# Optimization experiments

Hardware: AMD Instinct MI355X
Metric: run time of the kernel (lower is better)

Reference implementation:

```python
import jax, jax.numpy as jnp
import numpy as np

B, C_IN, C_OUT, DIRS, H, W = 16, 32, 32, 2, 64, 64


def setup_inputs() -> dict:
    key = jax.random.key(0)
    kx, kw = jax.random.split(key)
    x = jax.random.normal(kx, (B, C_IN, DIRS, H, W), dtype=jnp.float32)
    # xavier_normal_ on weight [O, C, C]: fan_in = C*C, fan_out = O*C
    std = float(np.sqrt(2.0 / (C_IN * C_IN + C_OUT * C_IN)))
    weight = jax.random.normal(kw, (C_OUT, C_IN, C_IN), dtype=jnp.float32) * std
    bias = jnp.zeros((C_OUT,), dtype=jnp.float32)
    return {"x": x, "weight": weight, "bias": bias}


def reference(x, weight, bias):
    # x: [B, C_in, dirs, H, W] real angles; z = exp(i*x)
    z = jax.lax.complex(jnp.cos(x), jnp.sin(x))  # complex64 [B,C,D,H,W]
    Wc = weight.astype(jnp.complex64)            # [O, C, C]
    # Per-pixel bilinear form: oc[b,o,d,h,w] = sum_{c,e} z[b,c] W[o,c,e] z[b,e]
    # (equivalent to the original full matmul + diagonal extraction)
    oc = jnp.einsum('oce,bcdhw,bedhw->bodhw', Wc, z, z)
    out = jnp.arctan2(oc.imag, oc.real)          # torch.angle
    return out + bias[None, :, None, None, None]
```

## Files before the change

kernel.cpp:

```cpp
#include <hip/hip_runtime.h>
#include <math.h>

typedef float        f32x2 __attribute__((ext_vector_type(2)));
typedef float        f32x4 __attribute__((ext_vector_type(4)));
typedef _Float16     f16x2 __attribute__((ext_vector_type(2)));
typedef _Float16     f16x8 __attribute__((ext_vector_type(8)));
typedef unsigned int u32;
typedef unsigned int u32x4 __attribute__((ext_vector_type(4)));

#define HW_    4096
#define CH_STR 8192
#define B_STR  262144
#define NPIX   131072
#define NKSTEP 20
#define NSLICE 80
#define NCT    84
#define NBEL   (NKSTEP*2*2*64*8)

#define WSCALE 512.0f
#define USCALE 1024.0f


__global__ void prep(const float* __restrict__ w,
                     _Float16* __restrict__ bfr,
                     u32* __restrict__ ct) {
    int idx = blockIdx.x * 256 + threadIdx.x;
    if (idx < NBEL) {
        int j    =  idx & 7;
        int lane = (idx >> 3) & 63;
        int frag = (idx >> 9) & 3;
        int ks   =  idx >> 11;
        int var  = frag >> 1;
        int oh   = frag & 1;
        int k = ks * 32 + ((lane >> 4) << 3) + j;
        int c = 0, base = 0;
        for (; c < 32; ++c) { int rl = 8 * ((c >> 3) + 1); if (k < base + rl) break; base += rl; }
        int e = k - base;
        int o = oh * 16 + (lane & 15);
        float v = 0.0f;
        if (e <= c)
            v = (e == c) ? w[o * 1024 + c * 33]
                         : (w[o * 1024 + c * 32 + e] + w[o * 1024 + e * 32 + c]);
        v *= WSCALE;
        _Float16 h = (_Float16)v;
        if (var) h = (_Float16)(v - (float)h);
        bfr[idx] = h;
    } else if (idx < NBEL + NCT) {
        int s = idx - NBEL;
        u32 v = 0;
        if (s < NSLICE) {
            int k = s * 8, c = 0, base = 0;
            for (; c < 32; ++c) { int rl = 8 * ((c >> 3) + 1); if (k < base + rl) break; base += rl; }
            v = ((u32)(c * 8) << 16) | (u32)((k - base) * 4);
        }
        ct[s] = v;
    }
}

#define TPB   256
#define TSTR  132

__device__ __forceinline__ f16x8 pack8(u32 a, u32 b, u32 c, u32 d) {
    u32x4 t = {a, b, c, d};
    return __builtin_bit_cast(f16x8, t);
}
__device__ __forceinline__ u32 pkrtz_u(float a, float b) {
    return __builtin_bit_cast(u32, __builtin_amdgcn_cvt_pkrtz(a, b));
}

__global__ __launch_bounds__(TPB, 4) void mfma_bilinear(
    const float* __restrict__ x,
    const _Float16* __restrict__ bfr,
    const u32* __restrict__ ct,
    const float* __restrict__ bias,
    float* __restrict__ out)
{
    __shared__ float trig[64 * TSTR];

    const int lane = threadIdx.x & 63;
    const int wv   = threadIdx.x >> 6;
    const int lg   = lane >> 4;
    const int lidm = lane & 15;
    const int P0   = blockIdx.x * 64;
    const int b    = P0 >> 13;
    const int d    = (P0 >> 12) & 1;
    const int hw0  = P0 & 4095;
    const int obase = b * B_STR + d * HW_ + hw0;

    const int px = wv * 16 + lidm;
    float* tp = trig + px * TSTR;
    const char* tb = (const char*)tp;

    #pragma unroll
    for (int m = 0; m < 8; ++m) {
        int c = lg * 8 + m;
        float xv = x[obase + px + c * CH_STR];
        float s, co; __sincosf(xv, &s, &co);
        *(f32x2*)(tp + 2 * c) = (f32x2){co * USCALE, s * USCALE};
        tp[64 + c] = co;
        tp[96 + c] = s;
    }

    f32x4 acc_r[2] = {{0.f,0.f,0.f,0.f}, {0.f,0.f,0.f,0.f}};
    f32x4 acc_i[2] = {{0.f,0.f,0.f,0.f}, {0.f,0.f,0.f,0.f}};

    const char* ubp = (const char*)bfr;
    const char* uct = (const char*)ct;
    const int lo16 = lane * 16;
    const int lg4  = lg * 4;

#define LDB(OFF)      (*(const f16x8*)(ubp + lo16 + (OFF)))
#define LDCT(OFF)     (*(const u32*)(uct + lg4 + (OFF)))
#define LOAD_TRIG(ST, CS, CE0, CE1, SE0, SE1) do { \
    const u32 st_ = (ST); \
    const int cB = (int)(st_ >> 16), eB = (int)(st_ & 0xffffu); \
    CS  = *(const f32x2*)(tb + cB); \
    CE0 = *(const f32x4*)(tb + 256 + eB); \
    CE1 = *(const f32x4*)(tb + 272 + eB); \
    SE0 = *(const f32x4*)(tb + 384 + eB); \
    SE1 = *(const f32x4*)(tb + 400 + eB); \
} while (0)

#define COMPUTE_STEP(CS, CE0, CE1, SE0, SE1, BH0, BH1, BL0, BL1) do { \
    const float ccs = (CS)[0]; \
    const float scs = (CS)[1]; \
    u32 hr[4], hi[4], lr[4], li[4]; \
    _Pragma("unroll") \
    for (int p = 0; p < 4; ++p) { \
        const float cea = (2*p     < 4) ? (CE0)[2*p]     : (CE1)[2*p - 4]; \
        const float sea = (2*p     < 4) ? (SE0)[2*p]     : (SE1)[2*p - 4]; \
        const float ceb = (2*p + 1 < 4) ? (CE0)[2*p + 1] : (CE1)[2*p - 3]; \
        const float seb = (2*p + 1 < 4) ? (SE0)[2*p + 1] : (SE1)[2*p - 3]; \
        const float ur0 = fmaf(ccs, cea, -(scs * sea)); \
        const float ui0 = fmaf(ccs, sea,   scs * cea); \
        const float ur1 = fmaf(ccs, ceb, -(scs * seb)); \
        const float ui1 = fmaf(ccs, seb,   scs * ceb); \
        hr[p] = pkrtz_u(ur0, ur1); \
        hi[p] = pkrtz_u(ui0, ui1); \
        const f16x2 h2r = __builtin_bit_cast(f16x2, hr[p]); \
        const f16x2 h2i = __builtin_bit_cast(f16x2, hi[p]); \
        lr[p] = pkrtz_u(ur0 - (float)h2r[0], ur1 - (float)h2r[1]); \
        li[p] = pkrtz_u(ui0 - (float)h2i[0], ui1 - (float)h2i[1]); \
    } \
    const f16x8 ahr = pack8(hr[0], hr[1], hr[2], hr[3]); \
    const f16x8 ahi = pack8(hi[0], hi[1], hi[2], hi[3]); \
    const f16x8 alr = pack8(lr[0], lr[1], lr[2], lr[3]); \
    const f16x8 ali = pack8(li[0], li[1], li[2], li[3]); \
    acc_r[0] = __builtin_amdgcn_mfma_f32_16x16x32_f16(ahr, BH0, acc_r[0], 0, 0, 0); \
    acc_i[0] = __builtin_amdgcn_mfma_f32_16x16x32_f16(ahi, BH0, acc_i[0], 0, 0, 0); \
    acc_r[1] = __builtin_amdgcn_mfma_f32_16x16x32_f16(ahr, BH1, acc_r[1], 0, 0, 0); \
    acc_i[1] = __builtin_amdgcn_mfma_f32_16x16x32_f16(ahi, BH1, acc_i[1], 0, 0, 0); \
    acc_r[0] = __builtin_amdgcn_mfma_f32_16x16x32_f16(ahr, BL0, acc_r[0], 0, 0, 0); \
    acc_i[0] = __builtin_amdgcn_mfma_f32_16x16x32_f16(ahi, BL0, acc_i[0], 0, 0, 0); \
    acc_r[1] = __builtin_amdgcn_mfma_f32_16x16x32_f16(ahr, BL1, acc_r[1], 0, 0, 0); \
    acc_i[1] = __builtin_amdgcn_mfma_f32_16x16x32_f16(ahi, BL1, acc_i[1], 0, 0, 0); \
    acc_r[0] = __builtin_amdgcn_mfma_f32_16x16x32_f16(alr, BH0, acc_r[0], 0, 0, 0); \
    acc_i[0] = __builtin_amdgcn_mfma_f32_16x16x32_f16(ali, BH0, acc_i[0], 0, 0, 0); \
    acc_r[1] = __builtin_amdgcn_mfma_f32_16x16x32_f16(alr, BH1, acc_r[1], 0, 0, 0); \
    acc_i[1] = __builtin_amdgcn_mfma_f32_16x16x32_f16(ali, BH1, acc_i[1], 0, 0, 0); \
} while (0)

    f16x8 bh0 = LDB(0), bh1 = LDB(1024), bl0 = LDB(2048), bl1 = LDB(3072);
    f32x2 cs; f32x4 ce0, ce1, se0, se1;
    LOAD_TRIG(LDCT(0), cs, ce0, ce1, se0, se1);
    u32 stN = LDCT(16);
    ubp += 4096;

    #pragma unroll 4
    for (int ks = 0; ks < NKSTEP - 1; ++ks) {
        f16x8 nbh0 = LDB(0), nbh1 = LDB(1024), nbl0 = LDB(2048), nbl1 = LDB(3072);
        f32x2 ncs; f32x4 nce0, nce1, nse0, nse1;
        LOAD_TRIG(stN, ncs, nce0, nce1, nse0, nse1);
        u32 stN2 = LDCT(32);

        COMPUTE_STEP(cs, ce0, ce1, se0, se1, bh0, bh1, bl0, bl1);

        bh0 = nbh0; bh1 = nbh1; bl0 = nbl0; bl1 = nbl1;
        cs = ncs; ce0 = nce0; ce1 = nce1; se0 = nse0; se1 = nse1;
        stN = stN2;
        ubp += 4096; uct += 16;
    }
    COMPUTE_STEP(cs, ce0, ce1, se0, se1, bh0, bh1, bl0, bl1);

    #pragma unroll
    for (int oh = 0; oh < 2; ++oh) {
        const int o = oh * 16 + lidm;
        const float bo = bias[o];
        #pragma unroll
        for (int q = 0; q < 4; ++q) {
            const int pxr = wv * 16 + lg * 4 + q;
            out[obase + pxr + o * CH_STR] = atan2f(acc_i[oh][q], acc_r[oh][q]) + bo;
        }
    }
#undef LDB
#undef LDCT
#undef LOAD_TRIG
#undef COMPUTE_STEP
}

extern "C" void kernel_launch(void* const* d_in, const int* in_sizes, int n_in,
                              void* d_out, int out_size, void* d_ws, size_t ws_size,
                              hipStream_t stream) {
    const float* x    = (const float*)d_in[0];
    const float* w    = (const float*)d_in[1];
    const float* bias = (const float*)d_in[2];
    float* out        = (float*)d_out;
    _Float16* bfr = (_Float16*)d_ws;
    u32*      ct  = (u32*)((char*)d_ws + 81920);

    {
        int n = NBEL + NCT;
        prep<<<(n + 255) / 256, 256, 0, stream>>>(w, bfr, ct);
    }
    {
        int grid = NPIX / 64;
        mfma_bilinear<<<grid, TPB, 0, stream>>>(x, bfr, ct, bias, out);
    }
}
```

Measured before the change: 53.58 us.

## Pack triangular weight rows in 4-wide chunks and compact the trig LDS table

```diff
diff --git a/kernel.cpp b/kernel.cpp
--- a/kernel.cpp
+++ b/kernel.cpp
@@ -6,16 +6,17 @@
 typedef _Float16     f16x2 __attribute__((ext_vector_type(2)));
 typedef _Float16     f16x8 __attribute__((ext_vector_type(8)));
 typedef unsigned int u32;
+typedef unsigned int u32x2 __attribute__((ext_vector_type(2)));
 typedef unsigned int u32x4 __attribute__((ext_vector_type(4)));
 
 #define HW_    4096
 #define CH_STR 8192
 #define B_STR  262144
 #define NPIX   131072
-#define NKSTEP 20
-#define NSLICE 80
-#define NCT    84
-#define NBEL   (NKSTEP*2*2*64*8)
+#define NKSTEP 18
+#define NSLICE 72
+#define NCT2   76
+#define NBEL   (NKSTEP*4*64*8)
 
 #define WSCALE 512.0f
 #define USCALE 1024.0f
@@ -23,7 +24,7 @@
 
 __global__ void prep(const float* __restrict__ w,
                      _Float16* __restrict__ bfr,
-                     u32* __restrict__ ct) {
+                     u32* __restrict__ ct2) {
     int idx = blockIdx.x * 256 + threadIdx.x;
     if (idx < NBEL) {
         int j    =  idx & 7;
@@ -34,7 +35,7 @@
         int oh   = frag & 1;
         int k = ks * 32 + ((lane >> 4) << 3) + j;
         int c = 0, base = 0;
-        for (; c < 32; ++c) { int rl = 8 * ((c >> 3) + 1); if (k < base + rl) break; base += rl; }
+        for (; c < 32; ++c) { int rl = ((c >> 2) + 1) << 2; if (k < base + rl) break; base += rl; }
         int e = k - base;
         int o = oh * 16 + (lane & 15);
         float v = 0.0f;
@@ -45,20 +46,21 @@
         _Float16 h = (_Float16)v;
         if (var) h = (_Float16)(v - (float)h);
         bfr[idx] = h;
-    } else if (idx < NBEL + NCT) {
-        int s = idx - NBEL;
+    } else if (idx < NBEL + 2 * NCT2) {
+        int t = idx - NBEL;
+        int s = t >> 1, half = t & 1;
         u32 v = 0;
         if (s < NSLICE) {
-            int k = s * 8, c = 0, base = 0;
-            for (; c < 32; ++c) { int rl = 8 * ((c >> 3) + 1); if (k < base + rl) break; base += rl; }
-            v = ((u32)(c * 8) << 16) | (u32)((k - base) * 4);
+            int k = s * 8 + half * 4, c = 0, base = 0;
+            for (; c < 32; ++c) { int rl = ((c >> 2) + 1) << 2; if (k < base + rl) break; base += rl; }
+            v = ((u32)(c * 8) << 16) | (u32)((k - base) * 8);
         }
-        ct[s] = v;
+        ct2[t] = v;
     }
 }
 
 #define TPB   256
-#define TSTR  132
+#define TSTR  67
 
 __device__ __forceinline__ f16x8 pack8(u32 a, u32 b, u32 c, u32 d) {
     u32x4 t = {a, b, c, d};
@@ -68,10 +70,10 @@
     return __builtin_bit_cast(u32, __builtin_amdgcn_cvt_pkrtz(a, b));
 }
 
-__global__ __launch_bounds__(TPB, 4) void mfma_bilinear(
+__global__ __launch_bounds__(TPB, 8) void mfma_bilinear(
     const float* __restrict__ x,
     const _Float16* __restrict__ bfr,
-    const u32* __restrict__ ct,
+    const u32* __restrict__ ct2,
     const float* __restrict__ bias,
     float* __restrict__ out)
 {
@@ -96,41 +98,41 @@
         int c = lg * 8 + m;
         float xv = x[obase + px + c * CH_STR];
         float s, co; __sincosf(xv, &s, &co);
-        *(f32x2*)(tp + 2 * c) = (f32x2){co * USCALE, s * USCALE};
-        tp[64 + c] = co;
-        tp[96 + c] = s;
+        *(f32x2*)(tb + 8 * c) = (f32x2){co, s};
     }
 
     f32x4 acc_r[2] = {{0.f,0.f,0.f,0.f}, {0.f,0.f,0.f,0.f}};
     f32x4 acc_i[2] = {{0.f,0.f,0.f,0.f}, {0.f,0.f,0.f,0.f}};
 
     const char* ubp = (const char*)bfr;
-    const char* uct = (const char*)ct;
+    const char* uct = (const char*)ct2;
     const int lo16 = lane * 16;
-    const int lg4  = lg * 4;
-
-#define LDB(OFF)      (*(const f16x8*)(ubp + lo16 + (OFF)))
-#define LDCT(OFF)     (*(const u32*)(uct + lg4 + (OFF)))
-#define LOAD_TRIG(ST, CS, CE0, CE1, SE0, SE1) do { \
-    const u32 st_ = (ST); \
-    const int cB = (int)(st_ >> 16), eB = (int)(st_ & 0xffffu); \
-    CS  = *(const f32x2*)(tb + cB); \
-    CE0 = *(const f32x4*)(tb + 256 + eB); \
-    CE1 = *(const f32x4*)(tb + 272 + eB); \
-    SE0 = *(const f32x4*)(tb + 384 + eB); \
-    SE1 = *(const f32x4*)(tb + 400 + eB); \
+    const int lg8  = lg * 8;
+
+#define LDB(OFF)   (*(const f16x8*)(ubp + lo16 + (OFF)))
+#define LDCT(OFF)  (*(const u32x2*)(uct + lg8 + (OFF)))
+#define LOAD_TRIG(ST, CS0, P00, P01, CS1, P10, P11) do { \
+    const u32x2 st_ = (ST); \
+    const int cB0 = (int)(st_.x >> 16), eB0 = (int)(st_.x & 0xffffu); \
+    const int cB1 = (int)(st_.y >> 16), eB1 = (int)(st_.y & 0xffffu); \
+    CS0 = *(const f32x2*)(tb + cB0); \
+    P00 = *(const f32x4*)(tb + eB0); \
+    P01 = *(const f32x4*)(tb + eB0 + 16); \
+    CS1 = *(const f32x2*)(tb + cB1); \
+    P10 = *(const f32x4*)(tb + eB1); \
+    P11 = *(const f32x4*)(tb + eB1 + 16); \
 } while (0)
 
-#define COMPUTE_STEP(CS, CE0, CE1, SE0, SE1, BH0, BH1, BL0, BL1) do { \
-    const float ccs = (CS)[0]; \
-    const float scs = (CS)[1]; \
+#define COMPUTE_STEP(CS0, P00, P01, CS1, P10, P11, BH0, BH1, BL0, BL1) do { \
+    const float cc0 = (CS0)[0] * USCALE, sc0 = (CS0)[1] * USCALE; \
+    const float cc1 = (CS1)[0] * USCALE, sc1 = (CS1)[1] * USCALE; \
     u32 hr[4], hi[4], lr[4], li[4]; \
     _Pragma("unroll") \
     for (int p = 0; p < 4; ++p) { \
-        const float cea = (2*p     < 4) ? (CE0)[2*p]     : (CE1)[2*p - 4]; \
-        const float sea = (2*p     < 4) ? (SE0)[2*p]     : (SE1)[2*p - 4]; \
-        const float ceb = (2*p + 1 < 4) ? (CE0)[2*p + 1] : (CE1)[2*p - 3]; \
-        const float seb = (2*p + 1 < 4) ? (SE0)[2*p + 1] : (SE1)[2*p - 3]; \
+        const f32x4 pe = (p == 0) ? (P00) : (p == 1) ? (P01) : (p == 2) ? (P10) : (P11); \
+        const float ccs = (p < 2) ? cc0 : cc1; \
+        const float scs = (p < 2) ? sc0 : sc1; \
+        const float cea = pe[0], sea = pe[1], ceb = pe[2], seb = pe[3]; \
         const float ur0 = fmaf(ccs, cea, -(scs * sea)); \
         const float ui0 = fmaf(ccs, sea,   scs * cea); \
         const float ur1 = fmaf(ccs, ceb, -(scs * seb)); \
@@ -161,26 +163,27 @@
 } while (0)
 
     f16x8 bh0 = LDB(0), bh1 = LDB(1024), bl0 = LDB(2048), bl1 = LDB(3072);
-    f32x2 cs; f32x4 ce0, ce1, se0, se1;
-    LOAD_TRIG(LDCT(0), cs, ce0, ce1, se0, se1);
-    u32 stN = LDCT(16);
+    f32x2 cs0, cs1; f32x4 p00, p01, p10, p11;
+    LOAD_TRIG(LDCT(0), cs0, p00, p01, cs1, p10, p11);
+    u32x2 stN = LDCT(32);
     ubp += 4096;
 
-    #pragma unroll 4
+    #pragma unroll 2
     for (int ks = 0; ks < NKSTEP - 1; ++ks) {
         f16x8 nbh0 = LDB(0), nbh1 = LDB(1024), nbl0 = LDB(2048), nbl1 = LDB(3072);
-        f32x2 ncs; f32x4 nce0, nce1, nse0, nse1;
-        LOAD_TRIG(stN, ncs, nce0, nce1, nse0, nse1);
-        u32 stN2 = LDCT(32);
-
-        COMPUTE_STEP(cs, ce0, ce1, se0, se1, bh0, bh1, bl0, bl1);
+        f32x2 ncs0, ncs1; f32x4 np00, np01, np10, np11;
+        LOAD_TRIG(stN, ncs0, np00, np01, ncs1, np10, np11);
+        u32x2 stN2 = LDCT(64);
+
+        COMPUTE_STEP(cs0, p00, p01, cs1, p10, p11, bh0, bh1, bl0, bl1);
 
         bh0 = nbh0; bh1 = nbh1; bl0 = nbl0; bl1 = nbl1;
-        cs = ncs; ce0 = nce0; ce1 = nce1; se0 = nse0; se1 = nse1;
+        cs0 = ncs0; cs1 = ncs1;
+        p00 = np00; p01 = np01; p10 = np10; p11 = np11;
         stN = stN2;
-        ubp += 4096; uct += 16;
-    }
-    COMPUTE_STEP(cs, ce0, ce1, se0, se1, bh0, bh1, bl0, bl1);
+        ubp += 4096; uct += 32;
+    }
+    COMPUTE_STEP(cs0, p00, p01, cs1, p10, p11, bh0, bh1, bl0, bl1);
 
     #pragma unroll
     for (int oh = 0; oh < 2; ++oh) {
@@ -206,14 +209,14 @@
     const float* bias = (const float*)d_in[2];
     float* out        = (float*)d_out;
     _Float16* bfr = (_Float16*)d_ws;
-    u32*      ct  = (u32*)((char*)d_ws + 81920);
+    u32*      ct2 = (u32*)((char*)d_ws + 73728);
 
     {
-        int n = NBEL + NCT;
-        prep<<<(n + 255) / 256, 256, 0, stream>>>(w, bfr, ct);
+        int n = NBEL + 2 * NCT2;
+        prep<<<(n + 255) / 256, 256, 0, stream>>>(w, bfr, ct2);
     }
     {
         int grid = NPIX / 64;
-        mfma_bilinear<<<grid, TPB, 0, stream>>>(x, bfr, ct, bias, out);
-    }
-}
+        mfma_bilinear<<<grid, TPB, 0, stream>>>(x, bfr, ct2, bias, out);
+    }
+}
```

Result: slower. 118.5 us (+121.2%).
